# Optimization experiments

Measured on AMD Instinct MI355X. Metric: run time of the kernel, lower is better.

The kernel has to match this reference:

```python
import jax, jax.numpy as jnp
import numpy as np
import math

NQ, NK, QDIM, MDIM, VDIM = 8192, 8192, 512, 512, 512
NEG = -float(1 << 32)


def setup_inputs() -> dict:
    key = jax.random.key(0)
    ks = jax.random.split(key, 8)
    Q = jax.random.normal(ks[0], (NQ, QDIM), dtype=jnp.float32)
    K = jax.random.normal(ks[1], (NK, QDIM), dtype=jnp.float32)
    V = jax.random.normal(ks[2], (NK, VDIM), dtype=jnp.float32)
    mask = jax.random.randint(ks[3], (NQ, NK), 0, 2) == 1
    s = 1.0 / math.sqrt(QDIM)
    WQ_w = jax.random.uniform(ks[4], (MDIM, QDIM), minval=-s, maxval=s, dtype=jnp.float32)
    WQ_b = jax.random.uniform(ks[5], (MDIM,), minval=-s, maxval=s, dtype=jnp.float32)
    WK_w = jax.random.uniform(ks[6], (MDIM, QDIM), minval=-s, maxval=s, dtype=jnp.float32)
    WK_b = jax.random.uniform(ks[7], (MDIM,), minval=-s, maxval=s, dtype=jnp.float32)
    return {"Q": Q, "K": K, "V": V, "WQ_w": WQ_w, "WQ_b": WQ_b,
            "WK_w": WK_w, "WK_b": WK_b, "mask": mask}


def reference(Q, K, V, WQ_w, WQ_b, WK_w, WK_b, mask):
    # Linear projections: y = x @ W^T + b
    Qp = Q @ WQ_w.T + WQ_b          # [NQ, MDIM]
    Kp = K @ WK_w.T + WK_b          # [NK, MDIM]
    scale = 1.0 / math.sqrt(MDIM)
    attn = (Qp @ Kp.T) * scale      # [NQ, NK]
    attn = jnp.where(mask, NEG, attn)
    attn = jax.nn.softmax(attn, axis=-1)
    return attn @ V                 # [NQ, VDIM]
```

## Files before the change

### kernel.cpp

```cpp
#include <hip/hip_runtime.h>

typedef __attribute__((ext_vector_type(8))) short short8;
typedef __attribute__((ext_vector_type(4))) float f32x4;

#define DEVFN __device__ __forceinline__

constexpr float SCALE_ATTN = 0.04419417382415922f;
constexpr float NEGF = -4294967296.0f;

DEVFN unsigned short f2bf(float f) {
  unsigned int u = __float_as_uint(f);
  u += 0x7FFFu + ((u >> 16) & 1u);
  return (unsigned short)(u >> 16);
}
DEVFN float bf2f(unsigned short h) { return __uint_as_float((unsigned)h << 16); }

DEVFN void gl_lds16(const void* g, void* l) {
  __builtin_amdgcn_global_load_lds(
      (const __attribute__((address_space(1))) unsigned int*)g,
      (__attribute__((address_space(3))) unsigned int*)l, 16, 0, 0);
}

__global__ void k_detect(const unsigned int* __restrict__ q, const unsigned int* __restrict__ m,
                         int* __restrict__ fflag, int* __restrict__ esize) {
  int lane = threadIdx.x;
  if (blockIdx.x == 0) {
    unsigned bad = 0;
    for (int i = 0; i < 64; i++) {
      unsigned v = q[i * 64 + lane];
      unsigned h = v & 0xFFFFu;
      unsigned e = (h >> 7) & 0xFFu;
      if (h != 0u && (e < 96u || e > 150u)) bad = 1;
    }
    unsigned long long anyb = __ballot(bad != 0);
    if (lane == 0) *fflag = (anyb == 0ULL) ? 1 : 0;
  } else {
    unsigned okd = 1, okh = 1, okb = 1;
    for (int i = 0; i < 64; i++) {
      unsigned v = m[i * 64 + lane];
      if (v > 1u && v != 0x3F800000u) okd = 0;
      unsigned h0 = v & 0xFFFFu, h1 = v >> 16;
      if ((h0 && h0 != 0x3F80u && h0 != 1u) || (h1 && h1 != 0x3F80u && h1 != 1u)) okh = 0;
      if (v & 0xFEFEFEFEu) okb = 0;
    }
    okd = (__ballot(okd == 0) == 0ULL);
    okh = (__ballot(okh == 0) == 0ULL);
    okb = (__ballot(okb == 0) == 0ULL);
    if (lane == 0) *esize = okd ? 4 : (okh ? 2 : 1);
  }
}

__global__ void k_prep(const void* __restrict__ Q, unsigned short* __restrict__ Qb,
                       const void* __restrict__ K, unsigned short* __restrict__ Kb,
                       const void* __restrict__ Wq, unsigned short* __restrict__ Wqb,
                       const void* __restrict__ Wk, unsigned short* __restrict__ Wkb,
                       const void* __restrict__ bq, unsigned short* __restrict__ bqb,
                       const void* __restrict__ bk, unsigned short* __restrict__ bkb,
                       const int* __restrict__ bf16flag) {
  int blk = blockIdx.x;
  const void* src; unsigned short* dst; int base, n;
  if (blk < 2048)      { src = Q;  dst = Qb;  base = blk;        n = 8192 * 512; }
  else if (blk < 4096) { src = K;  dst = Kb;  base = blk - 2048; n = 8192 * 512; }
  else if (blk < 4224) { src = Wq; dst = Wqb; base = blk - 4096; n = 512 * 512; }
  else if (blk < 4352) { src = Wk; dst = Wkb; base = blk - 4224; n = 512 * 512; }
  else if (blk == 4352){ src = bq; dst = bqb; base = 0;          n = 512; }
  else                 { src = bk; dst = bkb; base = 0;          n = 512; }
  int i = (base * 256 + threadIdx.x) * 8;
  if (i >= n) return;
  if (*bf16flag) {
    *(uint4*)(dst + i) = *(const uint4*)((const unsigned short*)src + i);
  } else {
    const float* f = (const float*)src + i;
    float4 a = *(const float4*)f, b = *(const float4*)(f + 4);
    uint4 o;
    o.x = (unsigned)f2bf(a.x) | ((unsigned)f2bf(a.y) << 16);
    o.y = (unsigned)f2bf(a.z) | ((unsigned)f2bf(a.w) << 16);
    o.z = (unsigned)f2bf(b.x) | ((unsigned)f2bf(b.y) << 16);
    o.w = (unsigned)f2bf(b.z) | ((unsigned)f2bf(b.w) << 16);
    *(uint4*)(dst + i) = o;
  }
}

__global__ void k_transpose_v(const void* __restrict__ Vsrc, const int* __restrict__ bf16flag,
                              unsigned short* __restrict__ Vt) {
  __shared__ unsigned short T[64][72];
  int t = threadIdx.x;
  int rb = blockIdx.x, cb = blockIdx.y;
  int r = t >> 3, c8 = (t & 7) * 8;
  int isbf = *bf16flag;
#pragma unroll
  for (int j = 0; j < 2; j++) {
    int row = rb * 64 + j * 32 + r;
    unsigned short e[8];
    if (isbf) {
      alignas(16) unsigned short tmp[8];
      *(uint4*)tmp = *(const uint4*)((const unsigned short*)Vsrc + (size_t)row * 512 + cb * 64 + c8);
#pragma unroll
      for (int i = 0; i < 8; i++) e[i] = tmp[i];
    } else {
      const float* f = (const float*)Vsrc + (size_t)row * 512 + cb * 64 + c8;
      float4 a = *(const float4*)f, b = *(const float4*)(f + 4);
      e[0] = f2bf(a.x); e[1] = f2bf(a.y); e[2] = f2bf(a.z); e[3] = f2bf(a.w);
      e[4] = f2bf(b.x); e[5] = f2bf(b.y); e[6] = f2bf(b.z); e[7] = f2bf(b.w);
    }
#pragma unroll
    for (int i = 0; i < 8; i++) T[c8 + i][j * 32 + r] = e[i];
  }
  __syncthreads();
#pragma unroll
  for (int j = 0; j < 2; j++) {
    int d = cb * 64 + j * 32 + r;
    alignas(16) unsigned short o[8];
#pragma unroll
    for (int i = 0; i < 8; i++) o[i] = T[j * 32 + r][c8 + i];
    int tt = rb * 2 + (c8 >> 5);
    *(uint4*)(Vt + ((size_t)tt * 512 + d) * 32 + (c8 & 31)) = *(const uint4*)o;
  }
}

DEVFN unsigned nib4(unsigned v) {
  unsigned t = v; t |= t >> 1; t |= t >> 2; t |= t >> 4; t &= 0x01010101u;
  return (t * 0x10204080u) >> 28;
}
DEVFN unsigned pair2(unsigned v) {
  unsigned t = v; t |= t >> 8; t |= t >> 4; t |= t >> 2; t |= t >> 1;
  return (t & 1u) | (((t >> 16) & 1u) << 1);
}
__global__ void k_pack(const void* __restrict__ mask, const int* __restrict__ esize,
                       unsigned long long* __restrict__ bits) {
  int wv = (blockIdx.x * blockDim.x + threadIdx.x) >> 6;
  int lane = threadIdx.x & 63;
  int sz = *esize;
  if (sz == 4) {
    const unsigned int* m = (const unsigned int*)mask;
    for (int g = wv; g < 262144; g += 4096) {
      size_t base = (size_t)g * 256 + lane;
      unsigned v0 = m[base], v1 = m[base + 64], v2 = m[base + 128], v3 = m[base + 192];
      unsigned long long b0 = __ballot(v0 != 0u);
      unsigned long long b1 = __ballot(v1 != 0u);
      unsigned long long b2 = __ballot(v2 != 0u);
      unsigned long long b3 = __ballot(v3 != 0u);
      if (lane == 0) {
        bits[g * 4 + 0] = b0; bits[g * 4 + 1] = b1;
        bits[g * 4 + 2] = b2; bits[g * 4 + 3] = b3;
      }
    }
  } else if (sz == 2) {
    const uint4* m = (const uint4*)mask;
    for (int g = wv; g < 131072; g += 4096) {
      uint4 v = m[(size_t)g * 64 + lane];
      unsigned c8 = pair2(v.x) | (pair2(v.y) << 2) | (pair2(v.z) << 4) | (pair2(v.w) << 6);
      unsigned long long x = (unsigned long long)c8 << ((lane & 7) * 8);
      x |= __shfl_xor(x, 1); x |= __shfl_xor(x, 2); x |= __shfl_xor(x, 4);
      if ((lane & 7) == 0) bits[g * 8 + (lane >> 3)] = x;
    }
  } else {
    const uint4* m = (const uint4*)mask;
    for (int g = wv; g < 65536; g += 4096) {
      uint4 v = m[(size_t)g * 64 + lane];
      unsigned c16 = nib4(v.x) | (nib4(v.y) << 4) | (nib4(v.z) << 8) | (nib4(v.w) << 12);
      unsigned long long x = (unsigned long long)c16 << ((lane & 3) * 16);
      x |= __shfl_xor(x, 1); x |= __shfl_xor(x, 2);
      if ((lane & 3) == 0) bits[g * 16 + (lane >> 2)] = x;
    }
  }
}

__global__ __launch_bounds__(256, 2) void k_proj(
    const unsigned short* __restrict__ Aq, const unsigned short* __restrict__ Wq,
    const unsigned short* __restrict__ bq, unsigned short* __restrict__ outq,
    const unsigned short* __restrict__ Ak, const unsigned short* __restrict__ Wk,
    const unsigned short* __restrict__ bk, unsigned short* __restrict__ outk) {
  const unsigned short* A = blockIdx.z ? Ak : Aq;
  const unsigned short* W = blockIdx.z ? Wk : Wq;
  const unsigned short* bias = blockIdx.z ? bk : bq;
  unsigned short* out = blockIdx.z ? outk : outq;

  __shared__ alignas(16) unsigned short As[128 * 64];
  __shared__ alignas(16) unsigned short Bs[128 * 64];
  int tid = threadIdx.x, lane = tid & 63, wave = tid >> 6;
  int wi = wave >> 1, wj = wave & 1;
  int l15 = lane & 15, l4 = lane >> 4;
  int rowbase = blockIdx.x * 128, colbase = blockIdx.y * 128;
  f32x4 acc[4][4];
#pragma unroll
  for (int i = 0; i < 4; i++)
#pragma unroll
    for (int j = 0; j < 4; j++) acc[i][j] = f32x4{0.f, 0.f, 0.f, 0.f};

  int swr = l15 & 7;
  for (int kb = 0; kb < 512; kb += 64) {
    __syncthreads();
#pragma unroll
    for (int t = 0; t < 4; t++) {
      int inst = wave * 4 + t;
      int r = inst * 8 + (lane >> 3);
      int c = ((lane & 7) ^ (r & 7)) * 8;
      gl_lds16(A + (size_t)(rowbase + r) * 512 + kb + c, &As[inst * 512]);
      gl_lds16(W + (size_t)(colbase + r) * 512 + kb + c, &Bs[inst * 512]);
    }
    __syncthreads();
#pragma unroll
    for (int t2 = 0; t2 < 2; t2++) {
      short8 a[4], b[4];
#pragma unroll
      for (int i = 0; i < 4; i++) {
        int row = wi * 64 + i * 16 + l15;
        a[i] = *(const short8*)&As[row * 64 + (((t2 * 4 + l4) ^ swr) * 8)];
      }
#pragma unroll
      for (int j = 0; j < 4; j++) {
        int row = wj * 64 + j * 16 + l15;
        b[j] = *(const short8*)&Bs[row * 64 + (((t2 * 4 + l4) ^ swr) * 8)];
      }
#pragma unroll
      for (int i = 0; i < 4; i++)
#pragma unroll
        for (int j = 0; j < 4; j++)
          acc[i][j] = __builtin_amdgcn_mfma_f32_16x16x32_bf16(a[i], b[j], acc[i][j], 0, 0, 0);
    }
  }
#pragma unroll
  for (int j = 0; j < 4; j++) {
    int col = colbase + wj * 64 + j * 16 + l15;
    float bj = bf2f(bias[col]);
#pragma unroll
    for (int i = 0; i < 4; i++) {
      int row0 = rowbase + wi * 64 + i * 16 + l4 * 4;
#pragma unroll
      for (int r = 0; r < 4; r++)
        out[(size_t)(row0 + r) * 512 + col] = f2bf(acc[i][j][r] + bj);
    }
  }
}

__global__ __launch_bounds__(512, 2) void k_attn(
    const unsigned short* __restrict__ Qp, const unsigned short* __restrict__ Kp,
    const unsigned short* __restrict__ Vt, const unsigned long long* __restrict__ mbits,
    unsigned short* __restrict__ Opart, float* __restrict__ mpart, float* __restrict__ lpart) {
  __shared__ alignas(16) unsigned short KB[16384];
  __shared__ alignas(16) unsigned short VB[16384];
  __shared__ alignas(16) unsigned short P[128 * 32];
  int tid = threadIdx.x, lane = tid & 63, wave = tid >> 6;
  int l15 = lane & 15, l4 = lane >> 4;
  int b = blockIdx.x;
  int split = b & 7;
  int qb = (b >> 3) * 128;

  short8 qf[16];
  {
    int row = qb + wave * 16 + l15;
#pragma unroll
    for (int t = 0; t < 16; t++)
      qf[t] = *(const short8*)(Qp + (size_t)row * 512 + t * 32 + l4 * 8);
  }
  f32x4 o[32];
#pragma unroll
  for (int f = 0; f < 32; f++) o[f] = f32x4{0.f, 0.f, 0.f, 0.f};
  float mi[4] = {NEGF, NEGF, NEGF, NEGF};
  float li[4] = {0.f, 0.f, 0.f, 0.f};

  int swK = l15 | ((l15 & 3) << 4);

  {
    int tv = split * 32;
#pragma unroll
    for (int t = 0; t < 4; t++) {
      int r = wave * 4 + t;
      int swz = (r & 15) | ((r & 3) << 4);
      gl_lds16(Kp + (size_t)(tv * 32 + r) * 512 + ((lane ^ swz) * 8), &KB[r * 512]);
    }
  }

  for (int it = 0; it < 32; it++) {
    int tv = split * 32 + it;
    unsigned long long mw[4];
#pragma unroll
    for (int r = 0; r < 4; r++)
      mw[r] = mbits[(size_t)(qb + wave * 16 + l4 * 4 + r) * 128 + split * 16 + (it >> 1)];
    int mshift = (it & 1) * 32;

    __syncthreads();

#pragma unroll
    for (int t = 0; t < 4; t++) {
      int inst = wave * 4 + t;
      int d = inst * 16 + (lane >> 2);
      int cg = (lane & 3) ^ (d & 3);
      gl_lds16(Vt + (size_t)tv * 16384 + d * 32 + cg * 8, &VB[inst * 512]);
    }

    f32x4 sacc[2];
#pragma unroll
    for (int c = 0; c < 2; c++) sacc[c] = f32x4{0.f, 0.f, 0.f, 0.f};
#pragma unroll
    for (int t2 = 0; t2 < 16; t2++) {
      short8 a = qf[t2];
#pragma unroll
      for (int c = 0; c < 2; c++) {
        int row = c * 16 + l15;
        short8 bb = *(const short8*)&KB[row * 512 + (((t2 * 4 + l4) ^ swK) * 8)];
        sacc[c] = __builtin_amdgcn_mfma_f32_16x16x32_bf16(a, bb, sacc[c], 0, 0, 0);
      }
    }

#pragma unroll
    for (int c = 0; c < 2; c++)
#pragma unroll
      for (int r = 0; r < 4; r++) {
        float s = sacc[c][r] * SCALE_ATTN;
        bool msk = (mw[r] >> (mshift + c * 16 + l15)) & 1ULL;
        sacc[c][r] = msk ? NEGF : s;
      }

    float alpha[4], mnew[4];
#pragma unroll
    for (int r = 0; r < 4; r++) {
      float t = fmaxf(sacc[0][r], sacc[1][r]);
#pragma unroll
      for (int off = 1; off < 16; off <<= 1) t = fmaxf(t, __shfl_xor(t, off, 64));
      float mn = fmaxf(mi[r], t);
      alpha[r] = __expf(mi[r] - mn);
      mi[r] = mn; mnew[r] = mn;
    }
#pragma unroll
    for (int c = 0; c < 2; c++)
#pragma unroll
      for (int r = 0; r < 4; r++)
        sacc[c][r] = __expf(sacc[c][r] - mnew[r]);
#pragma unroll
    for (int r = 0; r < 4; r++) {
      float t = sacc[0][r] + sacc[1][r];
#pragma unroll
      for (int off = 1; off < 16; off <<= 1) t += __shfl_xor(t, off, 64);
      li[r] = li[r] * alpha[r] + t;
    }

#pragma unroll
    for (int r = 0; r < 4; r++) {
      int prow = wave * 16 + l4 * 4 + r;
#pragma unroll
      for (int c = 0; c < 2; c++) {
        int chunk = (c * 2 + (l15 >> 3)) ^ (r & 3);
        P[prow * 32 + chunk * 8 + (l15 & 7)] = f2bf(sacc[c][r]);
      }
    }
#pragma unroll
    for (int f = 0; f < 32; f++)
#pragma unroll
      for (int r = 0; r < 4; r++) o[f][r] *= alpha[r];

    __syncthreads();

    {
      int tv1 = (it < 31) ? tv + 1 : tv;
#pragma unroll
      for (int t = 0; t < 4; t++) {
        int r = wave * 4 + t;
        int swz = (r & 15) | ((r & 3) << 4);
        gl_lds16(Kp + (size_t)(tv1 * 32 + r) * 512 + ((lane ^ swz) * 8), &KB[r * 512]);
      }
    }

    {
      int prow = wave * 16 + l15;
      short8 a = *(const short8*)&P[prow * 32 + ((l4 ^ (l15 & 3)) * 8)];
#pragma unroll
      for (int f = 0; f < 32; f++) {
        int d = f * 16 + l15;
        short8 bb = *(const short8*)&VB[d * 32 + ((l4 ^ (l15 & 3)) * 8)];
        o[f] = __builtin_amdgcn_mfma_f32_16x16x32_bf16(a, bb, o[f], 0, 0, 0);
      }
    }
  }

#pragma unroll
  for (int r = 0; r < 4; r++) {
    int row = qb + wave * 16 + l4 * 4 + r;
    if (l15 == 0) {
      mpart[(size_t)split * 8192 + row] = mi[r];
      lpart[(size_t)split * 8192 + row] = li[r];
    }
  }
  uint2* op = (uint2*)Opart;
#pragma unroll
  for (int f = 0; f < 32; f++) {
    uint2 v;
    v.x = (unsigned)f2bf(o[f][0]) | ((unsigned)f2bf(o[f][1]) << 16);
    v.y = (unsigned)f2bf(o[f][2]) | ((unsigned)f2bf(o[f][3]) << 16);
    op[((size_t)b * 32 + f) * 512 + tid] = v;
  }
}

__global__ void k_combine(const unsigned short* __restrict__ Opart,
                          const float* __restrict__ mpart, const float* __restrict__ lpart,
                          float* __restrict__ out) {
  int q = blockIdx.x;
  int half = blockIdx.y;
  int tid = threadIdx.x;
  int wave = tid >> 6, l4 = (tid >> 4) & 3, l15 = tid & 15;
  int row0 = q * 128 + wave * 16 + l4 * 4;

  float w[8][4], inv[4];
#pragma unroll
  for (int r = 0; r < 4; r++) {
    float M = NEGF;
    float mv[8];
#pragma unroll
    for (int s = 0; s < 8; s++) { mv[s] = mpart[s * 8192 + row0 + r]; M = fmaxf(M, mv[s]); }
    float L = 0.f;
#pragma unroll
    for (int s = 0; s < 8; s++) {
      float ws = __expf(mv[s] - M);
      w[s][r] = ws;
      L += ws * lpart[s * 8192 + row0 + r];
    }
    inv[r] = 1.0f / L;
  }
  const uint2* op = (const uint2*)Opart;
#pragma unroll
  for (int fo = 0; fo < 16; fo++) {
    int f = half * 16 + fo;
    float acc[4] = {0.f, 0.f, 0.f, 0.f};
#pragma unroll
    for (int s = 0; s < 8; s++) {
      uint2 v = op[((size_t)(q * 8 + s) * 32 + f) * 512 + tid];
      acc[0] += w[s][0] * bf2f((unsigned short)(v.x & 0xFFFFu));
      acc[1] += w[s][1] * bf2f((unsigned short)(v.x >> 16));
      acc[2] += w[s][2] * bf2f((unsigned short)(v.y & 0xFFFFu));
      acc[3] += w[s][3] * bf2f((unsigned short)(v.y >> 16));
    }
    int col = f * 16 + l15;
#pragma unroll
    for (int r = 0; r < 4; r++)
      out[(size_t)(row0 + r) * 512 + col] = acc[r] * inv[r];
  }
}

extern "C" void kernel_launch(void* const* d_in, const int* in_sizes, int n_in,
                              void* d_out, int out_size, void* d_ws, size_t ws_size,
                              hipStream_t stream) {
  const void* Q   = d_in[0];
  const void* K   = d_in[1];
  const void* V   = d_in[2];
  const void* WQw = d_in[3];
  const void* WQb = d_in[4];
  const void* WKw = d_in[5];
  const void* WKb = d_in[6];
  const void* mask = d_in[7];
  float* out = (float*)d_out;
  char* ws = (char*)d_ws;
  (void)in_sizes; (void)n_in; (void)out_size; (void)ws_size;

  constexpr size_t SZ_MAT = (size_t)8192 * 512 * 2;
  size_t off = 4096;
  unsigned short* Qb  = (unsigned short*)(ws + off); off += SZ_MAT;
  unsigned short* Kb  = (unsigned short*)(ws + off); off += SZ_MAT;
  unsigned short* Wqb = (unsigned short*)(ws + off); off += (size_t)512 * 512 * 2;
  unsigned short* Wkb = (unsigned short*)(ws + off); off += (size_t)512 * 512 * 2;
  unsigned short* bqb = (unsigned short*)(ws + off); off += 1024;
  unsigned short* bkb = (unsigned short*)(ws + off); off += 1024;
  unsigned short* Vt  = (unsigned short*)(ws + off); off += SZ_MAT;
  unsigned short* Qp  = (unsigned short*)(ws + off); off += SZ_MAT;
  unsigned short* Kp  = (unsigned short*)(ws + off); off += SZ_MAT;
  unsigned long long* mbits = (unsigned long long*)(ws + off); off += (size_t)8192 * 128 * 8;
  unsigned short* Opart = (unsigned short*)(ws + off); off += (size_t)512 * 512 * 32 * 8;
  float* mpart = (float*)(ws + off); off += (size_t)8 * 8192 * 4;
  float* lpart = (float*)(ws + off); off += (size_t)8 * 8192 * 4;
  int* fflag = (int*)ws;
  int* esize = (int*)(ws + 64);

  k_detect<<<2, 64, 0, stream>>>((const unsigned int*)Q, (const unsigned int*)mask, fflag, esize);
  k_prep<<<4354, 256, 0, stream>>>(Q, Qb, K, Kb, WQw, Wqb, WKw, Wkb, WQb, bqb, WKb, bkb, fflag);
  k_transpose_v<<<dim3(128, 8), 256, 0, stream>>>(V, fflag, Vt);
  k_pack<<<1024, 256, 0, stream>>>(mask, esize, mbits);
  k_proj<<<dim3(64, 4, 2), 256, 0, stream>>>(Qb, Wqb, bqb, Qp, Kb, Wkb, bkb, Kp);
  k_attn<<<512, 512, 0, stream>>>(Qp, Kp, Vt, mbits, Opart, mpart, lpart);
  k_combine<<<dim3(64, 2), 512, 0, stream>>>(Opart, mpart, lpart, out);
}
```

Measured before the change: 818.7 us.

## Split PV across waves by V columns, add lazy rescale and DPP reductions

Reorganizes the P·V stage so each wave owns 64 output columns for all 128 rows, loading its V fragments straight into registers instead of staging V through LDS. P is shared through LDS in a new layout, and the Opart layout and combine indexing change to match. Online-softmax rescaling now runs only when a row max grows by more than a threshold, with per-row alphas passed through LDS plus a block flag. Row reductions switch from shuffles to DPP. The aim is to cut LDS traffic and VALU rescale work, at the cost of extra LDS sync state and per-lane global V loads.

```diff
diff --git a/kernel.cpp b/kernel.cpp
--- a/kernel.cpp
+++ b/kernel.cpp
@@ -19,6 +19,31 @@
   __builtin_amdgcn_global_load_lds(
       (const __attribute__((address_space(1))) unsigned int*)g,
       (__attribute__((address_space(3))) unsigned int*)l, 16, 0, 0);
+}
+
+DEVFN float dpp_fmax16(float x) {
+  int v;
+  v = __builtin_amdgcn_update_dpp(0, __float_as_int(x), 0xB1, 0xF, 0xF, true);
+  x = fmaxf(x, __int_as_float(v));
+  v = __builtin_amdgcn_update_dpp(0, __float_as_int(x), 0x4E, 0xF, 0xF, true);
+  x = fmaxf(x, __int_as_float(v));
+  v = __builtin_amdgcn_update_dpp(0, __float_as_int(x), 0x141, 0xF, 0xF, true);
+  x = fmaxf(x, __int_as_float(v));
+  v = __builtin_amdgcn_update_dpp(0, __float_as_int(x), 0x140, 0xF, 0xF, true);
+  x = fmaxf(x, __int_as_float(v));
+  return x;
+}
+DEVFN float dpp_fadd16(float x) {
+  int v;
+  v = __builtin_amdgcn_update_dpp(0, __float_as_int(x), 0xB1, 0xF, 0xF, true);
+  x += __int_as_float(v);
+  v = __builtin_amdgcn_update_dpp(0, __float_as_int(x), 0x4E, 0xF, 0xF, true);
+  x += __int_as_float(v);
+  v = __builtin_amdgcn_update_dpp(0, __float_as_int(x), 0x141, 0xF, 0xF, true);
+  x += __int_as_float(v);
+  v = __builtin_amdgcn_update_dpp(0, __float_as_int(x), 0x140, 0xF, 0xF, true);
+  x += __int_as_float(v);
+  return x;
 }
 
 __global__ void k_detect(const unsigned int* __restrict__ q, const unsigned int* __restrict__ m,
@@ -239,8 +264,9 @@
     const unsigned short* __restrict__ Vt, const unsigned long long* __restrict__ mbits,
     unsigned short* __restrict__ Opart, float* __restrict__ mpart, float* __restrict__ lpart) {
   __shared__ alignas(16) unsigned short KB[16384];
-  __shared__ alignas(16) unsigned short VB[16384];
-  __shared__ alignas(16) unsigned short P[128 * 32];
+  __shared__ alignas(16) unsigned short P2[4][128][8];
+  __shared__ alignas(16) float alds[128];
+  __shared__ alignas(16) int nfl[8];
   int tid = threadIdx.x, lane = tid & 63, wave = tid >> 6;
   int l15 = lane & 15, l4 = lane >> 4;
   int b = blockIdx.x;
@@ -254,13 +280,16 @@
     for (int t = 0; t < 16; t++)
       qf[t] = *(const short8*)(Qp + (size_t)row * 512 + t * 32 + l4 * 8);
   }
-  f32x4 o[32];
-#pragma unroll
-  for (int f = 0; f < 32; f++) o[f] = f32x4{0.f, 0.f, 0.f, 0.f};
+  f32x4 o[8][4];
+#pragma unroll
+  for (int i = 0; i < 8; i++)
+#pragma unroll
+    for (int j = 0; j < 4; j++) o[i][j] = f32x4{0.f, 0.f, 0.f, 0.f};
   float mi[4] = {NEGF, NEGF, NEGF, NEGF};
   float li[4] = {0.f, 0.f, 0.f, 0.f};
 
   int swK = l15 | ((l15 & 3) << 4);
+  const unsigned int* mb32 = (const unsigned int*)mbits;
 
   {
     int tv = split * 32;
@@ -274,21 +303,17 @@
 
   for (int it = 0; it < 32; it++) {
     int tv = split * 32 + it;
-    unsigned long long mw[4];
+    unsigned mw[4];
 #pragma unroll
     for (int r = 0; r < 4; r++)
-      mw[r] = mbits[(size_t)(qb + wave * 16 + l4 * 4 + r) * 128 + split * 16 + (it >> 1)];
-    int mshift = (it & 1) * 32;
+      mw[r] = mb32[((size_t)(qb + wave * 16 + l4 * 4 + r) * 128 + split * 16 + (it >> 1)) * 2 + (it & 1)];
 
     __syncthreads();
 
-#pragma unroll
-    for (int t = 0; t < 4; t++) {
-      int inst = wave * 4 + t;
-      int d = inst * 16 + (lane >> 2);
-      int cg = (lane & 3) ^ (d & 3);
-      gl_lds16(Vt + (size_t)tv * 16384 + d * 32 + cg * 8, &VB[inst * 512]);
-    }
+    short8 vf[4];
+#pragma unroll
+    for (int df = 0; df < 4; df++)
+      vf[df] = *(const short8*)(Vt + ((size_t)tv * 512 + wave * 64 + df * 16 + l15) * 32 + l4 * 8);
 
     f32x4 sacc[2];
 #pragma unroll
@@ -309,46 +334,50 @@
 #pragma unroll
       for (int r = 0; r < 4; r++) {
         float s = sacc[c][r] * SCALE_ATTN;
-        bool msk = (mw[r] >> (mshift + c * 16 + l15)) & 1ULL;
+        bool msk = (mw[r] >> (c * 16 + l15)) & 1u;
         sacc[c][r] = msk ? NEGF : s;
       }
 
-    float alpha[4], mnew[4];
+    float al4[4];
+    bool need = false;
 #pragma unroll
     for (int r = 0; r < 4; r++) {
-      float t = fmaxf(sacc[0][r], sacc[1][r]);
-#pragma unroll
-      for (int off = 1; off < 16; off <<= 1) t = fmaxf(t, __shfl_xor(t, off, 64));
-      float mn = fmaxf(mi[r], t);
-      alpha[r] = __expf(mi[r] - mn);
-      mi[r] = mn; mnew[r] = mn;
-    }
+      float t = dpp_fmax16(fmaxf(sacc[0][r], sacc[1][r]));
+      al4[r] = t;
+      need |= (t > mi[r] + 8.0f);
+    }
+    unsigned long long blt = __ballot(need);
+    if (lane == 0) nfl[wave] = (blt != 0ULL) ? 1 : 0;
+    if (blt) {
+#pragma unroll
+      for (int r = 0; r < 4; r++) {
+        float mn = fmaxf(mi[r], al4[r]);
+        float a = __expf(mi[r] - mn);
+        li[r] *= a;
+        mi[r] = mn;
+        al4[r] = a;
+      }
+    } else {
+#pragma unroll
+      for (int r = 0; r < 4; r++) al4[r] = 1.0f;
+    }
+    if (l15 == 0) *(f32x4*)&alds[wave * 16 + l4 * 4] = f32x4{al4[0], al4[1], al4[2], al4[3]};
+
 #pragma unroll
     for (int c = 0; c < 2; c++)
 #pragma unroll
-      for (int r = 0; r < 4; r++)
-        sacc[c][r] = __expf(sacc[c][r] - mnew[r]);
-#pragma unroll
-    for (int r = 0; r < 4; r++) {
-      float t = sacc[0][r] + sacc[1][r];
-#pragma unroll
-      for (int off = 1; off < 16; off <<= 1) t += __shfl_xor(t, off, 64);
-      li[r] = li[r] * alpha[r] + t;
-    }
+      for (int r = 0; r < 4; r++) sacc[c][r] = __expf(sacc[c][r] - mi[r]);
+#pragma unroll
+    for (int r = 0; r < 4; r++)
+      li[r] += dpp_fadd16(sacc[0][r] + sacc[1][r]);
 
 #pragma unroll
     for (int r = 0; r < 4; r++) {
       int prow = wave * 16 + l4 * 4 + r;
 #pragma unroll
-      for (int c = 0; c < 2; c++) {
-        int chunk = (c * 2 + (l15 >> 3)) ^ (r & 3);
-        P[prow * 32 + chunk * 8 + (l15 & 7)] = f2bf(sacc[c][r]);
-      }
-    }
-#pragma unroll
-    for (int f = 0; f < 32; f++)
-#pragma unroll
-      for (int r = 0; r < 4; r++) o[f][r] *= alpha[r];
+      for (int c = 0; c < 2; c++)
+        P2[c * 2 + (l15 >> 3)][prow][l15 & 7] = f2bf(sacc[c][r]);
+    }
 
     __syncthreads();
 
@@ -363,14 +392,26 @@
     }
 
     {
-      int prow = wave * 16 + l15;
-      short8 a = *(const short8*)&P[prow * 32 + ((l4 ^ (l15 & 3)) * 8)];
-#pragma unroll
-      for (int f = 0; f < 32; f++) {
-        int d = f * 16 + l15;
-        short8 bb = *(const short8*)&VB[d * 32 + ((l4 ^ (l15 & 3)) * 8)];
-        o[f] = __builtin_amdgcn_mfma_f32_16x16x32_bf16(a, bb, o[f], 0, 0, 0);
-      }
+      const int4* n4 = (const int4*)nfl;
+      int4 na = n4[0], nb4 = n4[1];
+      if (na.x | na.y | na.z | na.w | nb4.x | nb4.y | nb4.z | nb4.w) {
+#pragma unroll
+        for (int rf = 0; rf < 8; rf++) {
+          f32x4 av = *(const f32x4*)&alds[rf * 16 + l4 * 4];
+#pragma unroll
+          for (int df = 0; df < 4; df++)
+#pragma unroll
+            for (int j = 0; j < 4; j++) o[rf][df][j] *= av[j];
+        }
+      }
+    }
+
+#pragma unroll
+    for (int rf = 0; rf < 8; rf++) {
+      short8 pa = *(const short8*)&P2[l4][rf * 16 + l15][0];
+#pragma unroll
+      for (int df = 0; df < 4; df++)
+        o[rf][df] = __builtin_amdgcn_mfma_f32_16x16x32_bf16(pa, vf[df], o[rf][df], 0, 0, 0);
     }
   }
 
@@ -382,14 +423,17 @@
       lpart[(size_t)split * 8192 + row] = li[r];
     }
   }
-  uint2* op = (uint2*)Opart;
-#pragma unroll
-  for (int f = 0; f < 32; f++) {
-    uint2 v;
-    v.x = (unsigned)f2bf(o[f][0]) | ((unsigned)f2bf(o[f][1]) << 16);
-    v.y = (unsigned)f2bf(o[f][2]) | ((unsigned)f2bf(o[f][3]) << 16);
-    op[((size_t)b * 32 + f) * 512 + tid] = v;
-  }
+  uint2* op2 = (uint2*)Opart;
+#pragma unroll
+  for (int rf = 0; rf < 8; rf++)
+#pragma unroll
+    for (int df = 0; df < 4; df++) {
+      int f = wave * 4 + df;
+      uint2 v;
+      v.x = (unsigned)f2bf(o[rf][df][0]) | ((unsigned)f2bf(o[rf][df][1]) << 16);
+      v.y = (unsigned)f2bf(o[rf][df][2]) | ((unsigned)f2bf(o[rf][df][3]) << 16);
+      op2[(((size_t)b * 32 + f) * 8 + rf) * 64 + l4 * 16 + l15] = v;
+    }
 }
 
 __global__ void k_combine(const unsigned short* __restrict__ Opart,
@@ -398,7 +442,7 @@
   int q = blockIdx.x;
   int half = blockIdx.y;
   int tid = threadIdx.x;
-  int wave = tid >> 6, l4 = (tid >> 4) & 3, l15 = tid & 15;
+  int wave = tid >> 6, lane = tid & 63, l4 = (lane >> 4) & 3, l15 = lane & 15;
   int row0 = q * 128 + wave * 16 + l4 * 4;
 
   float w[8][4], inv[4];
@@ -417,14 +461,14 @@
     }
     inv[r] = 1.0f / L;
   }
-  const uint2* op = (const uint2*)Opart;
+  const uint2* op2 = (const uint2*)Opart;
 #pragma unroll
   for (int fo = 0; fo < 16; fo++) {
     int f = half * 16 + fo;
     float acc[4] = {0.f, 0.f, 0.f, 0.f};
 #pragma unroll
     for (int s = 0; s < 8; s++) {
-      uint2 v = op[((size_t)(q * 8 + s) * 32 + f) * 512 + tid];
+      uint2 v = op2[(((size_t)(q * 8 + s) * 32 + f) * 8 + wave) * 64 + l4 * 16 + l15];
       acc[0] += w[s][0] * bf2f((unsigned short)(v.x & 0xFFFFu));
       acc[1] += w[s][1] * bf2f((unsigned short)(v.x >> 16));
       acc[2] += w[s][2] * bf2f((unsigned short)(v.y & 0xFFFFu));
```

Result: slower. 904.9 us (+10.5%).
